# Optimization experiments

Hardware: AMD Instinct MI355X
Metric: run time of the kernel (lower is better)

Reference implementation:

```python
import jax, jax.numpy as jnp
import numpy as np

N, E = 50000, 800000          # nodes, directed edges
IN_DIM, HC, OUT_DIM = 128, 64, 128
NEG_SLOPE = 0.2               # PyG GATConv default leaky_relu slope
EPS = 1e-5                    # PyG LayerNorm default eps


def setup_inputs() -> dict:
    key = jax.random.key(0)
    ks = jax.random.split(key, 10)
    s = 0.1
    return {
        "x": jax.random.normal(ks[0], (N, IN_DIM), jnp.float32),
        "edge_index": jax.random.randint(ks[1], (2, E), 0, N, dtype=jnp.int32),
        # conv1: GATConv(IN_DIM -> HC, heads=2, concat=True)
        "W1": jax.random.normal(ks[2], (IN_DIM, 2 * HC), jnp.float32) * s,
        "att_src1": jax.random.normal(ks[3], (2, HC), jnp.float32) * s,
        "att_dst1": jax.random.normal(ks[4], (2, HC), jnp.float32) * s,
        "b1": jnp.zeros((2 * HC,), jnp.float32),
        "ln1_w": jnp.ones((2 * HC,), jnp.float32),
        "ln1_b": jnp.zeros((2 * HC,), jnp.float32),
        # conv2: GATConv(2*HC -> OUT_DIM, heads=1, concat=False)
        "W2": jax.random.normal(ks[5], (2 * HC, OUT_DIM), jnp.float32) * s,
        "att_src2": jax.random.normal(ks[6], (1, OUT_DIM), jnp.float32) * s,
        "att_dst2": jax.random.normal(ks[7], (1, OUT_DIM), jnp.float32) * s,
        "b2": jnp.zeros((OUT_DIM,), jnp.float32),
        "ln2_w": jnp.ones((OUT_DIM,), jnp.float32),
        "ln2_b": jnp.zeros((OUT_DIM,), jnp.float32),
    }


def gat_conv(x, src, dst, W, att_src, att_dst, bias, heads, C, concat):
    """PyG GATConv (shared lin for src/dst, self-loops already in src/dst)."""
    n = x.shape[0]
    h = (x @ W).reshape(n, heads, C)                       # [N,H,C]
    a_src = jnp.einsum('nhc,hc->nh', h, att_src)           # [N,H]
    a_dst = jnp.einsum('nhc,hc->nh', h, att_dst)           # [N,H]
    e = jax.nn.leaky_relu(a_src[src] + a_dst[dst], NEG_SLOPE)   # [E',H]
    # numerically-stable softmax over incoming edges of each dst node
    emax = jax.ops.segment_max(e, dst, num_segments=n)     # [N,H] (self-loops => non-empty)
    ex = jnp.exp(e - emax[dst])
    denom = jax.ops.segment_sum(ex, dst, num_segments=n)
    alpha = ex / (denom[dst] + 1e-16)                      # [E',H]
    out = jax.ops.segment_sum(h[src] * alpha[:, :, None], dst, num_segments=n)  # [N,H,C]
    out = out.reshape(n, heads * C) if concat else out.mean(axis=1)
    return out + bias


def graph_layernorm(x, w, b):
    """PyG LayerNorm, mode='graph', single graph: normalize over ALL nodes+features."""
    mean = x.mean()
    xc = x - mean
    var = (xc * xc).mean()
    return xc * jax.lax.rsqrt(var + EPS) * w + b


def reference(x, edge_index, W1, att_src1, att_dst1, b1, ln1_w, ln1_b,
              W2, att_src2, att_dst2, b2, ln2_w, ln2_b):
    n = x.shape[0]
    loop = jnp.arange(n, dtype=edge_index.dtype)
    src = jnp.concatenate([edge_index[0], loop])           # add self-loops for GAT convs
    dst = jnp.concatenate([edge_index[1], loop])

    h = gat_conv(x, src, dst, W1, att_src1, att_dst1, b1, heads=2, C=HC, concat=True)
    h = jax.nn.relu(graph_layernorm(h, ln1_w, ln1_b))
    h = gat_conv(h, src, dst, W2, att_src2, att_dst2, b2, heads=1, C=OUT_DIM, concat=False)
    h = graph_layernorm(h, ln2_w, ln2_b)

    # SimpleConv(aggr='mean') over the ORIGINAL edges (no self-loops), then residual
    s0, d0 = edge_index[0], edge_index[1]
    agg = jax.ops.segment_sum(h[s0], d0, num_segments=n)
    cnt = jax.ops.segment_sum(jnp.ones(s0.shape, h.dtype), d0, num_segments=n)
    mean_agg = agg / jnp.maximum(cnt, 1.0)[:, None]
    return jax.nn.relu(mean_agg + x)
```

## Files before the change

### kernel.cpp

```cpp
#include <hip/hip_runtime.h>
#include <hip/hip_bf16.h>
#include <cstdint>
#include <cstddef>

#define NN 50000
#define EE 800000
#define DD 128
#define NEG 0.2f
#define EPSL 1e-5f

#define NB   196
#define EPB  4096
#define NBKT 196
#define HM   (NBKT * NB)
#define SCAP 7168

#define GROWS 64
#define AB    (NN / 8)

typedef __hip_bfloat16 bf16;
typedef short short8 __attribute__((ext_vector_type(8)));
typedef float f32x4 __attribute__((ext_vector_type(4)));

__device__ inline float bflo(unsigned u) { return __uint_as_float(u << 16); }
__device__ inline float bfhi(unsigned u) { return __uint_as_float(u & 0xffff0000u); }
__device__ inline float bf2f(unsigned short u) { return __uint_as_float((unsigned)u << 16); }

__device__ inline unsigned short f2bf(float f) {
    __bf16 h = (__bf16)f;
    return __builtin_bit_cast(unsigned short, h);
}
__device__ inline unsigned pack2(float a, float b) {
    return (unsigned)f2bf(a) | ((unsigned)f2bf(b) << 16);
}

__device__ inline void store4(float* Out, size_t idx, float4 v) {
    *(float4*)&Out[idx] = v;
}
__device__ inline void store4(bf16* Out, size_t idx, float4 v) {
    union { bf16 b[4]; ushort4 u; } cv;
    cv.b[0] = (bf16)v.x; cv.b[1] = (bf16)v.y; cv.b[2] = (bf16)v.z; cv.b[3] = (bf16)v.w;
    *(ushort4*)&Out[idx] = cv.u;
}


__global__ __launch_bounds__(256) void hist_kernel(const int* __restrict__ ei,
                                                   int* __restrict__ histG) {
    __shared__ int lh[NBKT];
    int tid = threadIdx.x;
    for (int t = tid; t < NBKT; t += 256) lh[t] = 0;
    __syncthreads();
    int base = blockIdx.x * EPB;
    #pragma unroll
    for (int j = 0; j < EPB / 1024; ++j) {
        int i4 = base + (j * 256 + tid) * 4;
        if (i4 < EE) {
            int4 d4 = *(const int4*)&ei[EE + i4];
            atomicAdd(&lh[(unsigned)d4.x >> 8], 1);
            atomicAdd(&lh[(unsigned)d4.y >> 8], 1);
            atomicAdd(&lh[(unsigned)d4.z >> 8], 1);
            atomicAdd(&lh[(unsigned)d4.w >> 8], 1);
        }
    }
    __syncthreads();
    for (int t = tid; t < NBKT; t += 256) histG[t * NB + blockIdx.x] = lh[t];
}

__global__ __launch_bounds__(1024) void scan_hist_kernel(const int* __restrict__ histG,
                                                         int* __restrict__ offs,
                                                         int* __restrict__ bstart) {
    __shared__ int wsum[16];
    __shared__ int carry_s;
    int tid = threadIdx.x, lane = tid & 63, wv = tid >> 6;
    if (tid == 0) carry_s = 0;
    __syncthreads();
    for (int base = 0; base < HM; base += 4096) {
        int i4 = base + tid * 4;
        int4 v = make_int4(0, 0, 0, 0);
        if (i4 + 3 < HM) v = *(const int4*)&histG[i4];
        else {
            if (i4 + 0 < HM) v.x = histG[i4 + 0];
            if (i4 + 1 < HM) v.y = histG[i4 + 1];
            if (i4 + 2 < HM) v.z = histG[i4 + 2];
            if (i4 + 3 < HM) v.w = histG[i4 + 3];
        }
        int tsum = v.x + v.y + v.z + v.w;
        int x = tsum;
        for (int off = 1; off < 64; off <<= 1) {
            int t = __shfl_up(x, off);
            if (lane >= off) x += t;
        }
        if (lane == 63) wsum[wv] = x;
        __syncthreads();
        if (wv == 0) {
            int s = (lane < 16) ? wsum[lane] : 0;
            for (int off = 1; off < 16; off <<= 1) {
                int t = __shfl_up(s, off);
                if (lane >= off) s += t;
            }
            if (lane < 16) wsum[lane] = s;
        }
        __syncthreads();
        int waveoff = (wv == 0) ? 0 : wsum[wv - 1];
        int carry = carry_s;
        int o0 = carry + waveoff + x - tsum;
        int o1 = o0 + v.x, o2 = o1 + v.y, o3 = o2 + v.z;
        if (i4 + 3 < HM) *(int4*)&offs[i4] = make_int4(o0, o1, o2, o3);
        else {
            if (i4 + 0 < HM) offs[i4 + 0] = o0;
            if (i4 + 1 < HM) offs[i4 + 1] = o1;
            if (i4 + 2 < HM) offs[i4 + 2] = o2;
            if (i4 + 3 < HM) offs[i4 + 3] = o3;
        }
        if (i4 < HM && (i4 % NB) == 0) bstart[i4 / NB] = o0;
        __syncthreads();
        if (tid == 0) carry_s += wsum[15];
        __syncthreads();
    }
    if (tid == 0) bstart[NBKT] = carry_s;
}

__global__ __launch_bounds__(512) void bucket_sort_kernel(const unsigned* __restrict__ tmp,
                                                          const int* __restrict__ bstart,
                                                          unsigned* __restrict__ col,
                                                          int* __restrict__ row_ptr) {
    __shared__ int cnt[256];
    __shared__ int cpos[256];
    __shared__ int wtot[4];
    __shared__ unsigned stage[SCAP];
    __shared__ unsigned sorted[SCAP];
    int tid = threadIdx.x, lane = tid & 63, wv = tid >> 6;
    int s0 = bstart[blockIdx.x], s1 = bstart[blockIdx.x + 1];
    int cntE = s1 - s0;
    bool lds_ok = (cntE <= SCAP);
    for (int t = tid; t < 256; t += 512) cnt[t] = 0;
    __syncthreads();
    if (lds_ok) {
        for (int i = tid; i < cntE; i += 512) {
            unsigned k = tmp[s0 + i];
            stage[i] = k;
            atomicAdd(&cnt[(k >> 16) & 0xFF], 1);
        }
    } else {
        for (int i = s0 + tid; i < s1; i += 512)
            atomicAdd(&cnt[(tmp[i] >> 16) & 0xFF], 1);
    }
    __syncthreads();
    int v = 0, x = 0;
    if (tid < 256) {
        v = cnt[tid];
        x = v;
        for (int off = 1; off < 64; off <<= 1) {
            int t = __shfl_up(x, off);
            if (lane >= off) x += t;
        }
        if (lane == 63) wtot[wv] = x;
    }
    __syncthreads();
    if (tid < 256) {
        int add = 0;
        for (int k = 0; k < wv; ++k) add += wtot[k];
        int start = s0 + add + x - v;
        cpos[tid] = start;
        int d = blockIdx.x * 256 + tid;
        if (d <= NN) row_ptr[d] = start;
    }
    __syncthreads();
    if (lds_ok) {
        for (int i = tid; i < cntE; i += 512) {
            unsigned key = stage[i];
            int pos = atomicAdd(&cpos[(key >> 16) & 0xFF], 1);
            sorted[pos - s0] = key;
        }
        __syncthreads();
        for (int i = tid; i < cntE; i += 512) col[s0 + i] = sorted[i];
    } else {
        for (int i = s0 + tid; i < s1; i += 512) {
            unsigned key = tmp[i];
            int pos = atomicAdd(&cpos[(key >> 16) & 0xFF], 1);
            col[pos] = key;
        }
    }
}

template <int H, bool LN, typename XT>
__device__ __forceinline__ void gemm_attn_body(int gb,
                                               const XT* __restrict__ X,
                                               const float* __restrict__ W,
                                               const float* __restrict__ att_s,
                                               const float* __restrict__ att_d,
                                               const float2* __restrict__ pstats,
                                               const float* __restrict__ lnw,
                                               const float* __restrict__ lnb,
                                               bf16* __restrict__ Hout,
                                               float* __restrict__ a_src,
                                               float* __restrict__ a_dst) {
    __shared__ __align__(16) char lds[(128 * 136 + 64 * 136) * 2 + 2048];
    unsigned short* Bt = (unsigned short*)lds;
    unsigned short* As = (unsigned short*)(lds + 128 * 136 * 2);
    float* Cs = (float*)lds;
    float* psum = (float*)(lds + (128 * 136 + 64 * 136) * 2);
    __shared__ double w1d[8], w2d[8], sred[2];

    int tid = threadIdx.x;
    int lane = tid & 63, w = tid >> 6;
    int row0 = gb * GROWS;

    double s1 = 0.0, s2 = 0.0;
    if (LN) {
        for (int i = tid; i < AB; i += 512) {
            float2 pv = pstats[i];
            s1 += (double)pv.x; s2 += (double)pv.y;
        }
    }

    {
        int c = tid & 127, kg = tid >> 7;
        #pragma unroll 2
        for (int i = 0; i < 8; ++i) {
            int k0 = i * 16 + kg * 4;
            float wa = W[(size_t)(k0 + 0) * DD + c];
            float wb = W[(size_t)(k0 + 1) * DD + c];
            float wcv = W[(size_t)(k0 + 2) * DD + c];
            float wdv = W[(size_t)(k0 + 3) * DD + c];
            uint2 pk = make_uint2(pack2(wa, wb), pack2(wcv, wdv));
            *(uint2*)&Bt[c * 136 + k0] = pk;
        }
    }

    if (LN) {
        #pragma unroll
        for (int off = 32; off; off >>= 1) {
            s1 += __shfl_xor(s1, off);
            s2 += __shfl_xor(s2, off);
        }
        if (lane == 0) { w1d[w] = s1; w2d[w] = s2; }
    }
    __syncthreads();
    if (LN && tid == 0) {
        double a = 0.0, b = 0.0;
        #pragma unroll
        for (int k = 0; k < 8; ++k) { a += w1d[k]; b += w2d[k]; }
        sred[0] = a; sred[1] = b;
    }
    __syncthreads();

    {
        int sub = tid & 31, rq = tid >> 5;
        int c4 = sub * 4;
        float mean = 0.f, inv = 1.f;
        float4 lw4 = make_float4(1.f, 1.f, 1.f, 1.f), lb4 = make_float4(0.f, 0.f, 0.f, 0.f);
        if (LN) {
            const double M = (double)NN * DD;
            double mean_d = sred[0] / M;
            double var_d = sred[1] / M - mean_d * mean_d;
            mean = (float)mean_d;
            inv = rsqrtf((float)var_d + EPSL);
            lw4 = *(const float4*)&lnw[c4];
            lb4 = *(const float4*)&lnb[c4];
        }
        #pragma unroll
        for (int i = 0; i < 4; ++i) {
            int r = i * 16 + rq;
            int row = row0 + r;
            float4 xv = make_float4(0.f, 0.f, 0.f, 0.f);
            if (row < NN) {
                if constexpr (sizeof(XT) == 4) {
                    xv = *(const float4*)&((const float*)X)[(size_t)row * DD + c4];
                } else {
                    ushort4 xb = *(const ushort4*)&((const unsigned short*)X)[(size_t)row * DD + c4];
                    xv = make_float4(bf2f(xb.x), bf2f(xb.y), bf2f(xb.z), bf2f(xb.w));
                }
            }
            if (LN) {
                xv.x = fmaxf((xv.x - mean) * inv * lw4.x + lb4.x, 0.f);
                xv.y = fmaxf((xv.y - mean) * inv * lw4.y + lb4.y, 0.f);
                xv.z = fmaxf((xv.z - mean) * inv * lw4.z + lb4.z, 0.f);
                xv.w = fmaxf((xv.w - mean) * inv * lw4.w + lb4.w, 0.f);
            }
            uint2 pk = make_uint2(pack2(xv.x, xv.y), pack2(xv.z, xv.w));
            *(uint2*)&As[r * 136 + c4] = pk;
        }
    }
    __syncthreads();

    int rg = w & 3, cg = w >> 2;
    int l15 = lane & 15, quad = lane >> 4;
    f32x4 acc[4];
    #pragma unroll
    for (int t = 0; t < 4; ++t) acc[t] = 0.f;
    const unsigned short* Arow = As + (rg * 16 + l15) * 136 + quad * 8;
    const unsigned short* Brow = Bt + l15 * 136 + quad * 8;
    #pragma unroll
    for (int ks = 0; ks < 4; ++ks) {
        short8 a = *(const short8*)(Arow + ks * 32);
        #pragma unroll
        for (int tt = 0; tt < 4; ++tt) {
            short8 b = *(const short8*)(Brow + (cg * 4 + tt) * 16 * 136 + ks * 32);
            acc[tt] = __builtin_amdgcn_mfma_f32_16x16x32_bf16(a, b, acc[tt], 0, 0, 0);
        }
    }
    __syncthreads();

    #pragma unroll
    for (int tt = 0; tt < 4; ++tt)
        #pragma unroll
        for (int r = 0; r < 4; ++r)
            Cs[(rg * 16 + quad * 4 + r) * 132 + (cg * 4 + tt) * 16 + l15] = acc[tt][r];

    float ds[4] = {0.f, 0.f, 0.f, 0.f}, dd[4] = {0.f, 0.f, 0.f, 0.f};
    #pragma unroll
    for (int tt = 0; tt < 4; ++tt) {
        int cc = (cg * 4 + tt) * 16 + l15;
        float as_ = att_s[cc], ad_ = att_d[cc];
        #pragma unroll
        for (int r = 0; r < 4; ++r) {
            ds[r] = fmaf(acc[tt][r], as_, ds[r]);
            dd[r] = fmaf(acc[tt][r], ad_, dd[r]);
        }
    }
    #pragma unroll
    for (int off = 1; off < 16; off <<= 1) {
        #pragma unroll
        for (int r = 0; r < 4; ++r) {
            ds[r] += __shfl_xor(ds[r], off);
            dd[r] += __shfl_xor(dd[r], off);
        }
    }
    if (l15 == 0) {
        #pragma unroll
        for (int r = 0; r < 4; ++r) {
            int rr = rg * 16 + quad * 4 + r;
            int row = row0 + rr;
            if (H == 2) {
                if (row < NN) {
                    a_src[row * 2 + cg] = ds[r];
                    a_dst[row * 2 + cg] = dd[r];
                }
            } else {
                psum[cg * 64 + rr] = ds[r];
                psum[128 + cg * 64 + rr] = dd[r];
            }
        }
    }
    __syncthreads();

    if (H == 1 && tid < 64) {
        int row = row0 + tid;
        if (row < NN) {
            a_src[row] = psum[tid] + psum[64 + tid];
            a_dst[row] = psum[128 + tid] + psum[192 + tid];
        }
    }

    {
        int sub = tid & 31, rq = tid >> 5;
        int c4 = sub * 4;
        unsigned short* Hp = (unsigned short*)Hout;
        #pragma unroll
        for (int i = 0; i < 4; ++i) {
            int r = i * 16 + rq;
            int row = row0 + r;
            if (row < NN) {
                float4 cv = *(const float4*)&Cs[r * 132 + c4];
                ushort4 pk;
                pk.x = f2bf(cv.x); pk.y = f2bf(cv.y);
                pk.z = f2bf(cv.z); pk.w = f2bf(cv.w);
                *(ushort4*)&Hp[(size_t)row * DD + c4] = pk;
            }
        }
    }
}

template <int H, bool LN, typename XT>
__global__ __launch_bounds__(512) void gemm_attn(const XT* __restrict__ X,
                                                 const float* __restrict__ W,
                                                 const float* __restrict__ att_s,
                                                 const float* __restrict__ att_d,
                                                 const float2* __restrict__ pstats,
                                                 const float* __restrict__ lnw,
                                                 const float* __restrict__ lnb,
                                                 bf16* __restrict__ Hout,
                                                 float* __restrict__ a_src,
                                                 float* __restrict__ a_dst) {
    gemm_attn_body<H, LN, XT>(blockIdx.x, X, W, att_s, att_d, pstats, lnw, lnb,
                              Hout, a_src, a_dst);
}

__global__ __launch_bounds__(512) void scatter_gemm1(const int* __restrict__ ei,
                                                     const int* __restrict__ offs,
                                                     unsigned* __restrict__ tmp,
                                                     const float* __restrict__ X,
                                                     const float* __restrict__ W,
                                                     const float* __restrict__ att_s,
                                                     const float* __restrict__ att_d,
                                                     bf16* __restrict__ Hout,
                                                     float* __restrict__ a_src,
                                                     float* __restrict__ a_dst) {
    if (blockIdx.x < NB) {
        __shared__ int lofs[NBKT];
        int tid = threadIdx.x;
        for (int t = tid; t < NBKT; t += 512) lofs[t] = offs[t * NB + blockIdx.x];
        __syncthreads();
        int base = blockIdx.x * EPB;
        #pragma unroll
        for (int j = 0; j < EPB / 2048; ++j) {
            int i4 = base + (j * 512 + tid) * 4;
            if (i4 < EE) {
                int4 s4 = *(const int4*)&ei[i4];
                int4 d4 = *(const int4*)&ei[EE + i4];
                unsigned k0 = ((unsigned)d4.x << 16) | (unsigned)s4.x;
                unsigned k1 = ((unsigned)d4.y << 16) | (unsigned)s4.y;
                unsigned k2 = ((unsigned)d4.z << 16) | (unsigned)s4.z;
                unsigned k3 = ((unsigned)d4.w << 16) | (unsigned)s4.w;
                tmp[atomicAdd(&lofs[(unsigned)d4.x >> 8], 1)] = k0;
                tmp[atomicAdd(&lofs[(unsigned)d4.y >> 8], 1)] = k1;
                tmp[atomicAdd(&lofs[(unsigned)d4.z >> 8], 1)] = k2;
                tmp[atomicAdd(&lofs[(unsigned)d4.w >> 8], 1)] = k3;
            }
        }
    } else {
        gemm_attn_body<2, false, float>(blockIdx.x - NB, X, W, att_s, att_d,
                                        nullptr, nullptr, nullptr, Hout, a_src, a_dst);
    }
}

template <int H, typename OT>
__global__ __launch_bounds__(256) void gat_agg(const int* __restrict__ row_ptr,
                                               const unsigned* __restrict__ col,
                                               const bf16* __restrict__ Hin,
                                               const float* __restrict__ a_src,
                                               const float* __restrict__ a_dst,
                                               const float* __restrict__ bias,
                                               OT* __restrict__ Out,
                                               float2* __restrict__ pstats) {
    int tid = threadIdx.x;
    int sl = tid & 31;
    int hw = tid >> 5;
    int n = blockIdx.x * 8 + hw;
    int c0 = sl * 4;
    const int head4 = (H == 2) ? (sl >> 4) : 0;

    int beg = row_ptr[n], end = row_ptr[n + 1];
    int deg = end - beg;

    float ad0 = a_dst[n * H + 0];
    float ad1 = (H == 2) ? a_dst[n * H + 1] : 0.f;
    const ushort* Hp = (const ushort*)Hin + c0;

    float acc[4] = {0.f, 0.f, 0.f, 0.f};
    float dl0 = 0.f, dl1 = 0.f;

    for (int base = 0; base < deg; base += 32) {
        int ecnt = min(32, deg - base);
        int sv = 0; float w0v = 0.f, w1v = 0.f;
        if (sl < ecnt) {
            sv = (int)(col[beg + base + sl] & 0xffffu);
            if (H == 2) {
                float2 av = *(const float2*)&a_src[sv * 2];
                float e0 = av.x + ad0; e0 = (e0 > 0.f) ? e0 : NEG * e0;
                float e1 = av.y + ad1; e1 = (e1 > 0.f) ? e1 : NEG * e1;
                w0v = __expf(e0); w1v = __expf(e1);
                dl0 += w0v; dl1 += w1v;
            } else {
                float e0 = a_src[sv] + ad0; e0 = (e0 > 0.f) ? e0 : NEG * e0;
                w0v = __expf(e0);
                dl0 += w0v;
            }
        }
        int j = 0;
        for (; j + 7 < ecnt; j += 8) {
            int s[8]; float ww[8];
            uint2 h[8];
            #pragma unroll
            for (int u = 0; u < 8; ++u) {
                s[u] = __shfl(sv, j + u, 32);
                if (H == 2) {
                    float a0 = __shfl(w0v, j + u, 32), b0 = __shfl(w1v, j + u, 32);
                    ww[u] = head4 ? b0 : a0;
                } else {
                    ww[u] = __shfl(w0v, j + u, 32);
                }
            }
            #pragma unroll
            for (int u = 0; u < 8; ++u) h[u] = *(const uint2*)(Hp + (size_t)s[u] * DD);
            #pragma unroll
            for (int u = 0; u < 8; ++u) {
                acc[0] = fmaf(ww[u], bflo(h[u].x), acc[0]);
                acc[1] = fmaf(ww[u], bfhi(h[u].x), acc[1]);
                acc[2] = fmaf(ww[u], bflo(h[u].y), acc[2]);
                acc[3] = fmaf(ww[u], bfhi(h[u].y), acc[3]);
            }
        }
        for (; j < ecnt; ++j) {
            int s = __shfl(sv, j, 32);
            float w;
            if (H == 2) {
                float a0 = __shfl(w0v, j, 32), b0 = __shfl(w1v, j, 32);
                w = head4 ? b0 : a0;
            } else {
                w = __shfl(w0v, j, 32);
            }
            uint2 hv = *(const uint2*)(Hp + (size_t)s * DD);
            acc[0] = fmaf(w, bflo(hv.x), acc[0]); acc[1] = fmaf(w, bfhi(hv.x), acc[1]);
            acc[2] = fmaf(w, bflo(hv.y), acc[2]); acc[3] = fmaf(w, bfhi(hv.y), acc[3]);
        }
    }

    #pragma unroll
    for (int off = 1; off < 32; off <<= 1) {
        dl0 += __shfl_xor(dl0, off);
        if (H == 2) dl1 += __shfl_xor(dl1, off);
    }

    float e0 = a_src[n * H + 0] + ad0; e0 = (e0 > 0.f) ? e0 : NEG * e0;
    float ws0 = __expf(e0);
    float ws1 = 0.f;
    if (H == 2) {
        float e1 = a_src[n * H + 1] + ad1; e1 = (e1 > 0.f) ? e1 : NEG * e1;
        ws1 = __expf(e1);
    }
    float den = (H == 2 && head4) ? (dl1 + ws1) : (dl0 + ws0);
    float wself = (H == 2 && head4) ? ws1 : ws0;
    float rinv = 1.f / (den + 1e-16f);
    uint2 hs = *(const uint2*)(Hp + (size_t)n * DD);
    float4 bi = *(const float4*)&bias[c0];
    float4 o;
    o.x = fmaf(wself, bflo(hs.x), acc[0]) * rinv + bi.x;
    o.y = fmaf(wself, bfhi(hs.x), acc[1]) * rinv + bi.y;
    o.z = fmaf(wself, bflo(hs.y), acc[2]) * rinv + bi.z;
    o.w = fmaf(wself, bfhi(hs.y), acc[3]) * rinv + bi.w;
    store4(Out, (size_t)n * DD + c0, o);

    float t1 = o.x + o.y + o.z + o.w;
    float t2 = o.x * o.x + o.y * o.y + o.z * o.z + o.w * o.w;
    #pragma unroll
    for (int off = 1; off < 32; off <<= 1) {
        t1 += __shfl_xor(t1, off);
        t2 += __shfl_xor(t2, off);
    }
    __shared__ float2 ps[8];
    if (sl == 0) ps[hw] = make_float2(t1, t2);
    __syncthreads();
    if (tid == 0) {
        float a = 0.f, b = 0.f;
        #pragma unroll
        for (int k = 0; k < 8; ++k) { a += ps[k].x; b += ps[k].y; }
        pstats[blockIdx.x] = make_float2(a, b);
    }
}

__global__ __launch_bounds__(1024) void reduce_stats_kernel(const float2* __restrict__ pstats,
                                                            double* __restrict__ stats) {
    int tid = threadIdx.x, lane = tid & 63, wv = tid >> 6;
    double s1 = 0.0, s2 = 0.0;
    for (int i = tid; i < AB; i += 1024) {
        float2 v = pstats[i];
        s1 += (double)v.x; s2 += (double)v.y;
    }
    for (int off = 32; off; off >>= 1) {
        s1 += __shfl_xor(s1, off);
        s2 += __shfl_xor(s2, off);
    }
    __shared__ double w1[16], w2[16];
    if (lane == 0) { w1[wv] = s1; w2[wv] = s2; }
    __syncthreads();
    if (tid == 0) {
        double a = 0.0, b = 0.0;
        for (int i = 0; i < 16; ++i) { a += w1[i]; b += w2[i]; }
        stats[0] = a; stats[1] = b;
    }
}

__global__ __launch_bounds__(256) void simpleconv_kernel(const int* __restrict__ row_ptr,
                                                         const unsigned* __restrict__ col,
                                                         const bf16* __restrict__ Hin,
                                                         const float* __restrict__ X,
                                                         const double* __restrict__ stats,
                                                         const float* __restrict__ lnw,
                                                         const float* __restrict__ lnb,
                                                         float* __restrict__ Out) {
    int tid = threadIdx.x;
    int sl = tid & 31;
    int n = blockIdx.x * 8 + (tid >> 5);
    int c0 = sl * 4;
    int beg = row_ptr[n], end = row_ptr[n + 1];
    int deg = end - beg;
    const ushort* Hp = (const ushort*)Hin + c0;

    float acc[4] = {0.f, 0.f, 0.f, 0.f};
    for (int base = 0; base < deg; base += 32) {
        int ecnt = min(32, deg - base);
        int sv = 0;
        if (sl < ecnt) sv = (int)(col[beg + base + sl] & 0xffffu);
        int j = 0;
        for (; j + 7 < ecnt; j += 8) {
            int s[8]; uint2 h[8];
            #pragma unroll
            for (int u = 0; u < 8; ++u) s[u] = __shfl(sv, j + u, 32);
            #pragma unroll
            for (int u = 0; u < 8; ++u) h[u] = *(const uint2*)(Hp + (size_t)s[u] * DD);
            #pragma unroll
            for (int u = 0; u < 8; ++u) {
                acc[0] += bflo(h[u].x); acc[1] += bfhi(h[u].x);
                acc[2] += bflo(h[u].y); acc[3] += bfhi(h[u].y);
            }
        }
        for (; j < ecnt; ++j) {
            int s = __shfl(sv, j, 32);
            uint2 hv = *(const uint2*)(Hp + (size_t)s * DD);
            acc[0] += bflo(hv.x); acc[1] += bfhi(hv.x);
            acc[2] += bflo(hv.y); acc[3] += bfhi(hv.y);
        }
    }

    const double M = (double)NN * DD;
    double mean_d = stats[0] / M;
    double var_d = stats[1] / M - mean_d * mean_d;
    float mean2 = (float)mean_d;
    float inv2 = rsqrtf((float)var_d + EPSL);
    float rc = 1.f / (float)((deg > 0) ? deg : 1);
    float4 xr = *(const float4*)&X[(size_t)n * DD + c0];
    float4 o;
    if (deg > 0) {
        float4 lw = *(const float4*)&lnw[c0];
        float4 lb = *(const float4*)&lnb[c0];
        o.x = (acc[0] * rc - mean2) * inv2 * lw.x + lb.x;
        o.y = (acc[1] * rc - mean2) * inv2 * lw.y + lb.y;
        o.z = (acc[2] * rc - mean2) * inv2 * lw.z + lb.z;
        o.w = (acc[3] * rc - mean2) * inv2 * lw.w + lb.w;
    } else {
        o.x = o.y = o.z = o.w = 0.f;
    }
    o.x = fmaxf(o.x + xr.x, 0.f);
    o.y = fmaxf(o.y + xr.y, 0.f);
    o.z = fmaxf(o.z + xr.z, 0.f);
    o.w = fmaxf(o.w + xr.w, 0.f);
    *(float4*)&Out[(size_t)n * DD + c0] = o;
}

extern "C" void kernel_launch(void* const* d_in, const int* in_sizes, int n_in,
                              void* d_out, int out_size, void* d_ws, size_t ws_size,
                              hipStream_t stream) {
    const float* x    = (const float*)d_in[0];
    const int*   ei   = (const int*)d_in[1];
    const float* W1   = (const float*)d_in[2];
    const float* as1  = (const float*)d_in[3];
    const float* ad1  = (const float*)d_in[4];
    const float* b1   = (const float*)d_in[5];
    const float* ln1w = (const float*)d_in[6];
    const float* ln1b = (const float*)d_in[7];
    const float* W2   = (const float*)d_in[8];
    const float* as2  = (const float*)d_in[9];
    const float* ad2  = (const float*)d_in[10];
    const float* b2   = (const float*)d_in[11];
    const float* ln2w = (const float*)d_in[12];
    const float* ln2b = (const float*)d_in[13];
    float* out = (float*)d_out;

    char* p = (char*)d_ws;
    auto alloc = [&](size_t bytes) {
        void* r = (void*)p;
        p += (bytes + 255) & ~(size_t)255;
        return r;
    };
    unsigned* tmp     = (unsigned*)alloc((size_t)EE * 4);
    unsigned* col     = (unsigned*)alloc((size_t)EE * 4);
    int*      histG   = (int*)alloc((size_t)HM * 4);
    int*      offs    = (int*)alloc((size_t)HM * 4);
    int*      bstart  = (int*)alloc((size_t)(NBKT + 1) * 4);
    int*      row_ptr = (int*)alloc((size_t)(NN + 256) * 4);
    double*   stats2  = (double*)alloc(16);
    float2*   pstats  = (float2*)alloc((size_t)AB * 8);
    bf16*     bufA    = (bf16*)alloc((size_t)NN * DD * 2);
    bf16*     bufB    = (bf16*)alloc((size_t)NN * DD * 2);
    float*    aS1     = (float*)alloc((size_t)NN * 2 * 4);
    float*    aD1     = (float*)alloc((size_t)NN * 2 * 4);
    float*    aS2     = (float*)alloc((size_t)NN * 4);
    float*    aD2     = (float*)alloc((size_t)NN * 4);

    const int GB = (NN + GROWS - 1) / GROWS;

    hist_kernel<<<NB, 256, 0, stream>>>(ei, histG);
    scan_hist_kernel<<<1, 1024, 0, stream>>>(histG, offs, bstart);
    scatter_gemm1<<<NB + GB, 512, 0, stream>>>(ei, offs, tmp,
                                               x, W1, as1, ad1, bufA, aS1, aD1);
    bucket_sort_kernel<<<NBKT, 512, 0, stream>>>(tmp, bstart, col, row_ptr);

    gat_agg<2, bf16><<<AB, 256, 0, stream>>>(row_ptr, col, bufA, aS1, aD1, b1, bufB, pstats);

    gemm_attn<1, true, bf16><<<GB, 512, 0, stream>>>(bufB, W2, as2, ad2,
                                                     pstats, ln1w, ln1b,
                                                     bufA, aS2, aD2);
    gat_agg<1, bf16><<<AB, 256, 0, stream>>>(row_ptr, col, bufA, aS2, aD2, b2, bufB, pstats);
    reduce_stats_kernel<<<1, 1024, 0, stream>>>(pstats, stats2);

    simpleconv_kernel<<<AB, 256, 0, stream>>>(row_ptr, col, bufB, x,
                                              stats2, ln2w, ln2b, out);
}
```

Baseline: 266.5 us.

## Unroll gather loops by 16 with padded lanes and use fewer, larger histogram blocks

The GAT and mean aggregation loops now gather 16 neighbor rows per iteration instead of 8, and the scalar tail loop is gone. Padded lanes carry zero weight, or source 0 with a zero multiplier, so more loads are in flight per wave. Separately, the edge histogram and scatter stages now use 64 blocks of 12544 edges instead of 196 blocks of 4096, which shrinks the histogram matrix that must be scanned. The trade-offs are wasted loads and FMAs on padded entries for low-degree nodes, and less parallelism in the histogram and scatter kernels.

```diff
diff --git a/kernel.cpp b/kernel.cpp
--- a/kernel.cpp
+++ b/kernel.cpp
@@ -9,8 +9,8 @@
 #define NEG 0.2f
 #define EPSL 1e-5f
 
-#define NB   196
-#define EPB  4096
+#define NB   64
+#define EPB  12544
 #define NBKT 196
 #define HM   (NBKT * NB)
 #define SCAP 7168
@@ -52,14 +52,17 @@
     __syncthreads();
     int base = blockIdx.x * EPB;
     #pragma unroll
-    for (int j = 0; j < EPB / 1024; ++j) {
-        int i4 = base + (j * 256 + tid) * 4;
-        if (i4 < EE) {
-            int4 d4 = *(const int4*)&ei[EE + i4];
-            atomicAdd(&lh[(unsigned)d4.x >> 8], 1);
-            atomicAdd(&lh[(unsigned)d4.y >> 8], 1);
-            atomicAdd(&lh[(unsigned)d4.z >> 8], 1);
-            atomicAdd(&lh[(unsigned)d4.w >> 8], 1);
+    for (int j = 0; j < (EPB + 1023) / 1024; ++j) {
+        int off = (j * 256 + tid) * 4;
+        if (off < EPB) {
+            int i4 = base + off;
+            if (i4 < EE) {
+                int4 d4 = *(const int4*)&ei[EE + i4];
+                atomicAdd(&lh[(unsigned)d4.x >> 8], 1);
+                atomicAdd(&lh[(unsigned)d4.y >> 8], 1);
+                atomicAdd(&lh[(unsigned)d4.z >> 8], 1);
+                atomicAdd(&lh[(unsigned)d4.w >> 8], 1);
+            }
         }
     }
     __syncthreads();
@@ -404,19 +407,22 @@
         __syncthreads();
         int base = blockIdx.x * EPB;
         #pragma unroll
-        for (int j = 0; j < EPB / 2048; ++j) {
-            int i4 = base + (j * 512 + tid) * 4;
-            if (i4 < EE) {
-                int4 s4 = *(const int4*)&ei[i4];
-                int4 d4 = *(const int4*)&ei[EE + i4];
-                unsigned k0 = ((unsigned)d4.x << 16) | (unsigned)s4.x;
-                unsigned k1 = ((unsigned)d4.y << 16) | (unsigned)s4.y;
-                unsigned k2 = ((unsigned)d4.z << 16) | (unsigned)s4.z;
-                unsigned k3 = ((unsigned)d4.w << 16) | (unsigned)s4.w;
-                tmp[atomicAdd(&lofs[(unsigned)d4.x >> 8], 1)] = k0;
-                tmp[atomicAdd(&lofs[(unsigned)d4.y >> 8], 1)] = k1;
-                tmp[atomicAdd(&lofs[(unsigned)d4.z >> 8], 1)] = k2;
-                tmp[atomicAdd(&lofs[(unsigned)d4.w >> 8], 1)] = k3;
+        for (int j = 0; j < (EPB + 2047) / 2048; ++j) {
+            int off = (j * 512 + tid) * 4;
+            if (off < EPB) {
+                int i4 = base + off;
+                if (i4 < EE) {
+                    int4 s4 = *(const int4*)&ei[i4];
+                    int4 d4 = *(const int4*)&ei[EE + i4];
+                    unsigned k0 = ((unsigned)d4.x << 16) | (unsigned)s4.x;
+                    unsigned k1 = ((unsigned)d4.y << 16) | (unsigned)s4.y;
+                    unsigned k2 = ((unsigned)d4.z << 16) | (unsigned)s4.z;
+                    unsigned k3 = ((unsigned)d4.w << 16) | (unsigned)s4.w;
+                    tmp[atomicAdd(&lofs[(unsigned)d4.x >> 8], 1)] = k0;
+                    tmp[atomicAdd(&lofs[(unsigned)d4.y >> 8], 1)] = k1;
+                    tmp[atomicAdd(&lofs[(unsigned)d4.z >> 8], 1)] = k2;
+                    tmp[atomicAdd(&lofs[(unsigned)d4.w >> 8], 1)] = k3;
+                }
             }
         }
     } else {
@@ -468,13 +474,15 @@
                 dl0 += w0v;
             }
         }
-        int j = 0;
-        for (; j + 7 < ecnt; j += 8) {
-            int s[8]; float ww[8];
-            uint2 h[8];
+        int ecnt16 = (ecnt + 15) & ~15;
+        for (int j = 0; j < ecnt16; j += 16) {
+            int s[16]; uint2 h[16]; float ww[16];
             #pragma unroll
-            for (int u = 0; u < 8; ++u) {
-                s[u] = __shfl(sv, j + u, 32);
+            for (int u = 0; u < 16; ++u) s[u] = __shfl(sv, j + u, 32);
+            #pragma unroll
+            for (int u = 0; u < 16; ++u) h[u] = *(const uint2*)(Hp + (size_t)s[u] * DD);
+            #pragma unroll
+            for (int u = 0; u < 16; ++u) {
                 if (H == 2) {
                     float a0 = __shfl(w0v, j + u, 32), b0 = __shfl(w1v, j + u, 32);
                     ww[u] = head4 ? b0 : a0;
@@ -483,27 +491,12 @@
                 }
             }
             #pragma unroll
-            for (int u = 0; u < 8; ++u) h[u] = *(const uint2*)(Hp + (size_t)s[u] * DD);
-            #pragma unroll
-            for (int u = 0; u < 8; ++u) {
+            for (int u = 0; u < 16; ++u) {
                 acc[0] = fmaf(ww[u], bflo(h[u].x), acc[0]);
                 acc[1] = fmaf(ww[u], bfhi(h[u].x), acc[1]);
                 acc[2] = fmaf(ww[u], bflo(h[u].y), acc[2]);
                 acc[3] = fmaf(ww[u], bfhi(h[u].y), acc[3]);
             }
-        }
-        for (; j < ecnt; ++j) {
-            int s = __shfl(sv, j, 32);
-            float w;
-            if (H == 2) {
-                float a0 = __shfl(w0v, j, 32), b0 = __shfl(w1v, j, 32);
-                w = head4 ? b0 : a0;
-            } else {
-                w = __shfl(w0v, j, 32);
-            }
-            uint2 hv = *(const uint2*)(Hp + (size_t)s * DD);
-            acc[0] = fmaf(w, bflo(hv.x), acc[0]); acc[1] = fmaf(w, bfhi(hv.x), acc[1]);
-            acc[2] = fmaf(w, bflo(hv.y), acc[2]); acc[3] = fmaf(w, bfhi(hv.y), acc[3]);
         }
     }
 
@@ -593,24 +586,21 @@
         int ecnt = min(32, deg - base);
         int sv = 0;
         if (sl < ecnt) sv = (int)(col[beg + base + sl] & 0xffffu);
-        int j = 0;
-        for (; j + 7 < ecnt; j += 8) {
-            int s[8]; uint2 h[8];
+        int ecnt16 = (ecnt + 15) & ~15;
+        for (int j = 0; j < ecnt16; j += 16) {
+            int s[16]; uint2 h[16];
             #pragma unroll
-            for (int u = 0; u < 8; ++u) s[u] = __shfl(sv, j + u, 32);
+            for (int u = 0; u < 16; ++u) s[u] = __shfl(sv, j + u, 32);
             #pragma unroll
-            for (int u = 0; u < 8; ++u) h[u] = *(const uint2*)(Hp + (size_t)s[u] * DD);
+            for (int u = 0; u < 16; ++u) h[u] = *(const uint2*)(Hp + (size_t)s[u] * DD);
             #pragma unroll
-            for (int u = 0; u < 8; ++u) {
-                acc[0] += bflo(h[u].x); acc[1] += bfhi(h[u].x);
-                acc[2] += bflo(h[u].y); acc[3] += bfhi(h[u].y);
-            }
-        }
-        for (; j < ecnt; ++j) {
-            int s = __shfl(sv, j, 32);
-            uint2 hv = *(const uint2*)(Hp + (size_t)s * DD);
-            acc[0] += bflo(hv.x); acc[1] += bfhi(hv.x);
-            acc[2] += bflo(hv.y); acc[3] += bfhi(hv.y);
+            for (int u = 0; u < 16; ++u) {
+                float ww = (j + u < ecnt) ? 1.f : 0.f;
+                acc[0] = fmaf(ww, bflo(h[u].x), acc[0]);
+                acc[1] = fmaf(ww, bfhi(h[u].x), acc[1]);
+                acc[2] = fmaf(ww, bflo(h[u].y), acc[2]);
+                acc[3] = fmaf(ww, bfhi(h[u].y), acc[3]);
+            }
         }
     }
 
```

After: 265.2 us. Within noise of the previous version (-0.5%).
